# Performance work log

Hardware: AMD Instinct MI355X
Metric: run time of the kernel (lower is better)

The kernel has to match this reference:

```python
import jax, jax.numpy as jnp
import numpy as np

N_STEP = 64
GAMMA = 10.0
DIST_MIN, DIST_MAX = 0.0, 10.0
N_LAYER = 4
H_DIM, E_DIM, HID_DIM = 128, 16, 256
N_NODES, N_EDGES = 10000, 320000


def setup_inputs() -> dict:
    key = jax.random.key(0)
    ks = jax.random.split(key, 12)
    in_m = 2 * H_DIM + E_DIM + N_STEP  # 336
    s = 0.02
    return {
        "x": jax.random.normal(ks[0], (N_NODES, H_DIM), jnp.float32),
        "pos": jax.random.normal(ks[1], (N_NODES, 3), jnp.float32),
        "edge_index": jax.random.randint(ks[2], (2, N_EDGES), 0, N_NODES),
        "edge_attr": jax.random.normal(ks[3], (N_EDGES, E_DIM), jnp.float32),
        "Wm": jax.random.normal(ks[4], (N_LAYER, in_m, HID_DIM), jnp.float32) * s,
        "bm": jnp.zeros((N_LAYER, HID_DIM), jnp.float32),
        "Wp": jax.random.normal(ks[5], (N_LAYER, HID_DIM, 1), jnp.float32) * s,
        "bp": jnp.zeros((N_LAYER, 1), jnp.float32),
        "Wx": jax.random.normal(ks[6], (N_LAYER, H_DIM + HID_DIM, H_DIM), jnp.float32) * s,
        "bx": jnp.zeros((N_LAYER, H_DIM), jnp.float32),
    }


def _egnn_layer(x, pos, edge_index, edge_attr, Wm, bm, Wp, bp, Wx, bx):
    i, j = edge_index[0], edge_index[1]
    n = x.shape[0]
    x_i, x_j = x[i], x[j]                       # [E, h] gathers
    # NOTE: source uses x (not pos) for the distance feature -- replicated.
    r = jnp.linalg.norm(x_i - x_j, axis=1)      # [E]
    c = jnp.linspace(DIST_MIN, DIST_MAX, N_STEP, dtype=x.dtype)
    soh = jnp.exp(-GAMMA * (r[:, None] - c[None, :]) ** 2)  # [E, n_step]
    m_ij = jnp.concatenate([x_i, x_j, soh, edge_attr], axis=1) @ Wm + bm  # [E, hid]
    _alpha = m_ij @ Wp + bp  # computed but unused in source's _update_pos
    # position update: scatter-mean of pos_i - pos_j over destination i
    pos_vect = pos[i] - pos[j]                  # [E, 3]
    cnt = jax.ops.segment_sum(jnp.ones((i.shape[0],), pos.dtype), i, num_segments=n)
    pos_aggr = jax.ops.segment_sum(pos_vect, i, num_segments=n) / jnp.maximum(cnt, 1.0)[:, None]
    pos = pos + pos_aggr
    # feature update: scatter-sum of messages
    m_aggr = jax.ops.segment_sum(m_ij, i, num_segments=n)  # [N, hid]
    x = jnp.concatenate([x, m_aggr], axis=1) @ Wx + bx      # [N, h]
    return x, pos


def reference(x, pos, edge_index, edge_attr, Wm, bm, Wp, bp, Wx, bx):
    x_ori = x
    for l in range(N_LAYER):
        x, pos = _egnn_layer(x, pos, edge_index, edge_attr,
                             Wm[l], bm[l], Wp[l], bp[l], Wx[l], bx[l])
        x = jax.nn.leaky_relu(x)
    x = x_ori + x            # residual_connection == 'add'
    x = jax.nn.leaky_relu(x)  # activate_last
    return x, pos
```

## Files before the change

### kernel.cpp

```cpp
#include <hip/hip_runtime.h>
#include <hip/hip_bf16.h>

#define NN 10000
#define NE 320000
#define HD 128
#define ED 16
#define HID 256
#define KP 480
#define AST 488

typedef unsigned short ushort_t;
typedef __attribute__((ext_vector_type(8))) short short8;
typedef __attribute__((ext_vector_type(4))) float f32x4;

__device__ __forceinline__ float leaky(float v){ return v > 0.f ? v : 0.01f*v; }
__device__ __forceinline__ ushort_t f2bs(float v){
  __hip_bfloat16 b = __float2bfloat16(v);
  return *(ushort_t*)&b;
}
__device__ __forceinline__ unsigned pack2u(float a, float b){
  return (unsigned)f2bs(a) | ((unsigned)f2bs(b) << 16);
}
__device__ __forceinline__ float bl(unsigned u){ return __uint_as_float(u << 16); }
__device__ __forceinline__ float bh(unsigned u){ return __uint_as_float(u & 0xffff0000u); }
__device__ __forceinline__ float2 cvt2(unsigned u){ return make_float2(bl(u), bh(u)); }

__global__ __launch_bounds__(256) void k_misc(const float* __restrict__ x, ushort_t* __restrict__ xb,
                                              const int* __restrict__ ii, int* __restrict__ cnt,
                                              const float* __restrict__ Wx, ushort_t* __restrict__ WcT){
  int t = blockIdx.x*256 + threadIdx.x;
  if (t < NN*HD){
    xb[t] = f2bs(x[t]);
  } else if (t < NN*HD + NE){
    atomicAdd(&cnt[ii[t - NN*HD]], 1);
  } else if (t < NN*HD + NE + 4*HD*HD){
    int u = t - NN*HD - NE;
    int l = u >> 14, r = (u >> 7) & 127, c = u & 127;
    WcT[((long)l*HD + c)*KP + r] = f2bs(Wx[(long)l*(HD+HID)*HD + r*HD + c]);
  } else {
    int u = t - NN*HD - NE - 4*HD*HD;
    if (u < 4*HD*15){
      int row = u / 15, k = 465 + u % 15;
      WcT[(long)row*KP + k] = 0;
    }
  }
}

__global__ __launch_bounds__(256) void k_scan(const int* __restrict__ cnt, int* __restrict__ row_ptr){
  const int PER = 40;
  __shared__ int sh[256];
  int t = threadIdx.x;
  int base = t*PER;
  int s = 0;
  for (int k = 0; k < PER; ++k){ int idx = base+k; if (idx < NN) s += cnt[idx]; }
  sh[t] = s; __syncthreads();
  for (int off = 1; off < 256; off <<= 1){
    int v = (t >= off) ? sh[t-off] : 0;
    __syncthreads();
    sh[t] += v;
    __syncthreads();
  }
  int pre = sh[t] - s;
  for (int k = 0; k < PER; ++k){
    int idx = base+k;
    if (idx < NN){ row_ptr[idx] = pre; pre += cnt[idx]; }
  }
  if (t == 255) row_ptr[NN] = sh[255];
}

__global__ __launch_bounds__(256) void k_fillwc(const int* __restrict__ ii, const int* __restrict__ jj,
                                                const int* __restrict__ row_ptr, int* __restrict__ c2,
                                                int* __restrict__ sj, int* __restrict__ se,
                                                const float* __restrict__ Wm, const float* __restrict__ bm,
                                                const float* __restrict__ Wx, ushort_t* __restrict__ WcT){
  if (blockIdx.x < 1250){
    int e = blockIdx.x*256 + threadIdx.x;
    int a = ii[e];
    int p = atomicAdd(&c2[a], 1);
    int idx = row_ptr[a] + p;
    sj[idx] = jj[e];
    se[idx] = e;
    return;
  }
  __shared__ float a_s[16*36];
  __shared__ float w_s[16*128];
  int bi = blockIdx.x - 1250;
  int t  = threadIdx.x;
  int rb = (bi % 11) * 32;
  int l  = bi / 11;
  int lr = t >> 4, lk = t & 15;
  int wcc = t & 127, wk = t >> 7;
  int cg = t & 31, rg = t >> 5;
  const float* Wxb = Wx + (long)l*(HD+HID)*HD + HD*HD;
  float acc[4][4];
  #pragma unroll
  for (int i = 0; i < 4; ++i)
    #pragma unroll
    for (int j = 0; j < 4; ++j) acc[i][j] = 0.f;
  for (int k0 = 0; k0 < HID; k0 += 16){
    int m0 = rb + lr, m1 = rb + lr + 16;
    float v0 = 0.f, v1 = 0.f;
    if (m0 < 336) v0 = Wm[((long)l*336 + m0)*HID + k0 + lk];
    else if (m0 == 336) v0 = bm[l*HID + k0 + lk];
    if (m1 < 336) v1 = Wm[((long)l*336 + m1)*HID + k0 + lk];
    else if (m1 == 336) v1 = bm[l*HID + k0 + lk];
    a_s[lk*36 + lr]      = v0;
    a_s[lk*36 + lr + 16] = v1;
    #pragma unroll
    for (int q = 0; q < 8; ++q)
      w_s[(wk + 2*q)*128 + wcc] = Wxb[(k0 + wk + 2*q)*HD + wcc];
    __syncthreads();
    #pragma unroll
    for (int k = 0; k < 16; ++k){
      float4 av = *(const float4*)&a_s[k*36 + rg*4];
      float4 wv = *(const float4*)&w_s[k*128 + cg*4];
      acc[0][0] += av.x*wv.x; acc[0][1] += av.x*wv.y; acc[0][2] += av.x*wv.z; acc[0][3] += av.x*wv.w;
      acc[1][0] += av.y*wv.x; acc[1][1] += av.y*wv.y; acc[1][2] += av.y*wv.z; acc[1][3] += av.y*wv.w;
      acc[2][0] += av.z*wv.x; acc[2][1] += av.z*wv.y; acc[2][2] += av.z*wv.z; acc[2][3] += av.z*wv.w;
      acc[3][0] += av.w*wv.x; acc[3][1] += av.w*wv.y; acc[3][2] += av.w*wv.z; acc[3][3] += av.w*wv.w;
    }
    __syncthreads();
  }
  #pragma unroll
  for (int i = 0; i < 4; ++i){
    int m = rb + rg*4 + i;
    if (m < 337){
      #pragma unroll
      for (int j = 0; j < 4; ++j)
        WcT[((long)l*HD + cg*4 + j)*KP + 128 + m] = f2bs(acc[i][j]);
    }
  }
}

template<int FIRST, int FINAL>
__global__ __launch_bounds__(256) void k_layer(const uint4* __restrict__ xb4, const float* __restrict__ posf_cur,
                                               const int* __restrict__ row_ptr, const int* __restrict__ sj,
                                               const int* __restrict__ se, const float* __restrict__ ea,
                                               ushort_t* __restrict__ inv,
                                               const ushort_t* __restrict__ WcT, const float* __restrict__ bx,
                                               ushort_t* __restrict__ xb_next, const float* __restrict__ x_ori,
                                               float* __restrict__ out, float* __restrict__ posf_next){
  __shared__ ushort_t Asm[8*AST];
  int tid = threadIdx.x;
  int nl  = tid >> 5;
  int n   = blockIdx.x*8 + nl;
  int sub = tid & 31;
  int g   = sub >> 4;
  int gl  = sub & 15;
  int beg = row_ptr[n], end = row_ptr[n+1];
  int len = end - beg;
  int q0 = beg + ((len * g) >> 1);
  int q1 = beg + ((len * (g+1)) >> 1);

  uint4 xi = xb4[(long)n*16 + gl];
  float2 xi0 = cvt2(xi.x), xi1 = cvt2(xi.y), xi2 = cvt2(xi.z), xi3 = cvt2(xi.w);
  float c0 = (10.0f/63.0f)*(float)(4*gl);
  float c1 = (10.0f/63.0f)*(float)(4*gl+1);
  float c2 = (10.0f/63.0f)*(float)(4*gl+2);
  float c3 = (10.0f/63.0f)*(float)(4*gl+3);

  float2 s0 = {0,0}, s1 = {0,0}, s2 = {0,0}, s3 = {0,0};
  float h0 = 0, h1 = 0, h2 = 0, h3 = 0, sp = 0, sea = 0;

#define EPROC(Bv, Jv, Ev) { \
    float2 e0=cvt2(Bv.x), e1=cvt2(Bv.y), e2=cvt2(Bv.z), e3=cvt2(Bv.w); \
    float d, p=0.f; \
    d=xi0.x-e0.x; p+=d*d;  d=xi0.y-e0.y; p+=d*d; \
    d=xi1.x-e1.x; p+=d*d;  d=xi1.y-e1.y; p+=d*d; \
    d=xi2.x-e2.x; p+=d*d;  d=xi2.y-e2.y; p+=d*d; \
    d=xi3.x-e3.x; p+=d*d;  d=xi3.y-e3.y; p+=d*d; \
    p += __shfl_xor(p,1,64); p += __shfl_xor(p,2,64); \
    p += __shfl_xor(p,4,64); p += __shfl_xor(p,8,64); \
    float r = sqrtf(p); \
    float t0=r-c0, t1=r-c1, t2=r-c2, t3=r-c3; \
    h0 += __expf(-10.f*t0*t0); h1 += __expf(-10.f*t1*t1); \
    h2 += __expf(-10.f*t2*t2); h3 += __expf(-10.f*t3*t3); \
    s0.x+=e0.x; s0.y+=e0.y; s1.x+=e1.x; s1.y+=e1.y; \
    s2.x+=e2.x; s2.y+=e2.y; s3.x+=e3.x; s3.y+=e3.y; \
    if (FIRST) sea += ea[(long)(Ev)*ED + gl]; \
    if (gl < 3) sp += posf_cur[(long)Jv*3 + gl]; }

  int idx = q0;
  for (; idx + 3 < q1; idx += 4){
    int j0 = sj[idx], j1 = sj[idx+1], j2 = sj[idx+2], j3 = sj[idx+3];
    int e0i = FIRST ? se[idx]   : 0;
    int e1i = FIRST ? se[idx+1] : 0;
    int e2i = FIRST ? se[idx+2] : 0;
    int e3i = FIRST ? se[idx+3] : 0;
    uint4 B0 = xb4[(long)j0*16 + gl];
    uint4 B1 = xb4[(long)j1*16 + gl];
    uint4 B2 = xb4[(long)j2*16 + gl];
    uint4 B3 = xb4[(long)j3*16 + gl];
    EPROC(B0, j0, e0i); EPROC(B1, j1, e1i); EPROC(B2, j2, e2i); EPROC(B3, j3, e3i);
  }
  for (; idx < q1; ++idx){
    int j0 = sj[idx];
    int e0i = FIRST ? se[idx] : 0;
    uint4 B0 = xb4[(long)j0*16 + gl];
    EPROC(B0, j0, e0i);
  }
#undef EPROC

  s0.x += __shfl_xor(s0.x,16,64); s0.y += __shfl_xor(s0.y,16,64);
  s1.x += __shfl_xor(s1.x,16,64); s1.y += __shfl_xor(s1.y,16,64);
  s2.x += __shfl_xor(s2.x,16,64); s2.y += __shfl_xor(s2.y,16,64);
  s3.x += __shfl_xor(s3.x,16,64); s3.y += __shfl_xor(s3.y,16,64);
  h0 += __shfl_xor(h0,16,64); h1 += __shfl_xor(h1,16,64);
  h2 += __shfl_xor(h2,16,64); h3 += __shfl_xor(h3,16,64);
  sp += __shfl_xor(sp,16,64);
  if (FIRST) sea += __shfl_xor(sea,16,64);

  if (g == 0){
    float cf = (float)len;
    ushort_t* Ar = Asm + nl*AST;
    ((uint4*)Ar)[gl] = xi;
    ((uint4*)(Ar + 128))[gl] = make_uint4(pack2u(cf*xi0.x, cf*xi0.y), pack2u(cf*xi1.x, cf*xi1.y),
                                          pack2u(cf*xi2.x, cf*xi2.y), pack2u(cf*xi3.x, cf*xi3.y));
    ((uint4*)(Ar + 256))[gl] = make_uint4(pack2u(s0.x, s0.y), pack2u(s1.x, s1.y),
                                          pack2u(s2.x, s2.y), pack2u(s3.x, s3.y));
    ((uint2*)(Ar + 384))[gl] = make_uint2(pack2u(h0, h1), pack2u(h2, h3));
    ushort_t sea_us;
    if (FIRST){
      sea_us = f2bs(sea);
      inv[(long)n*16 + gl] = sea_us;
    } else {
      sea_us = inv[(long)n*16 + gl];
    }
    Ar[448 + gl] = sea_us;
    Ar[464 + gl] = (gl == 0) ? f2bs(cf) : (ushort_t)0;
    if (gl < 3){
      float pi = posf_cur[n*3 + gl];
      posf_next[n*3 + gl] = pi + (cf*pi - sp) / fmaxf(cf, 1.f);
    }
  }
  __syncthreads();

  int wave = tid >> 6, lane = tid & 63;
  int quad = lane >> 4, l16 = lane & 15;
  int nb = wave * 32;
  const ushort_t* Arow = Asm + (l16 & 7)*AST + quad*8;
  const ushort_t* W0 = WcT + (long)(nb + l16)*KP + quad*8;
  const ushort_t* W1 = WcT + (long)(nb + 16 + l16)*KP + quad*8;
  f32x4 acc0 = {0,0,0,0}, acc1 = {0,0,0,0};
  for (int k0 = 0; k0 < KP; k0 += 32){
    short8 av = *(const short8*)(Arow + k0);
    short8 b0 = *(const short8*)(W0 + k0);
    short8 b1 = *(const short8*)(W1 + k0);
    acc0 = __builtin_amdgcn_mfma_f32_16x16x32_bf16(av, b0, acc0, 0, 0, 0);
    acc1 = __builtin_amdgcn_mfma_f32_16x16x32_bf16(av, b1, acc1, 0, 0, 0);
  }
  float bx0 = bx[nb + l16], bx1 = bx[nb + 16 + l16];
  #pragma unroll
  for (int r = 0; r < 4; ++r){
    int row = quad*4 + r;
    if (row < 8){
      long base = (long)(blockIdx.x*8 + row)*HD;
      float v0 = leaky(acc0[r] + bx0);
      float v1 = leaky(acc1[r] + bx1);
      if (FINAL){
        out[base + nb + l16]      = leaky(x_ori[base + nb + l16] + v0);
        out[base + nb + 16 + l16] = leaky(x_ori[base + nb + 16 + l16] + v1);
      } else {
        xb_next[base + nb + l16]      = f2bs(v0);
        xb_next[base + nb + 16 + l16] = f2bs(v1);
      }
    }
  }
}

extern "C" void kernel_launch(void* const* d_in, const int* in_sizes, int n_in,
                              void* d_out, int out_size, void* d_ws, size_t ws_size,
                              hipStream_t stream){
  const float* x   = (const float*)d_in[0];
  const float* pos = (const float*)d_in[1];
  const int*   ei  = (const int*)d_in[2];
  const float* ea  = (const float*)d_in[3];
  const float* Wm  = (const float*)d_in[4];
  const float* bm  = (const float*)d_in[5];
  const float* Wx  = (const float*)d_in[8];
  const float* bx  = (const float*)d_in[9];
  float* out_x   = (float*)d_out;
  float* out_pos = out_x + NN*HD;

  ushort_t* xbA    = (ushort_t*)d_ws;
  ushort_t* xbB    = xbA + NN*HD;
  ushort_t* WcT    = xbB + NN*HD;
  ushort_t* inv    = WcT + 4*HD*KP;
  float*    pfA    = (float*)(inv + NN*16);
  float*    pfB    = pfA + NN*3;
  int*      cnt    = (int*)(pfB + NN*3);
  int*      c2     = cnt + NN;
  int*      row_ptr= c2 + NN;
  int*      sj     = row_ptr + (NN+1);
  int*      se     = sj + NE;
  const int* ii = ei;
  const int* jj = ei + NE;

  hipMemsetAsync(cnt, 0, 2*NN*sizeof(int), stream);
  int misc_threads = NN*HD + NE + 4*HD*HD + 4*HD*15;
  k_misc  <<<(misc_threads + 255)/256, 256, 0, stream>>>(x, xbA, ii, cnt, Wx, WcT);
  k_scan  <<<1, 256, 0, stream>>>(cnt, row_ptr);
  k_fillwc<<<1250 + 44, 256, 0, stream>>>(ii, jj, row_ptr, c2, sj, se, Wm, bm, Wx, WcT);

  const float* ps[4] = {pos, pfA, pfB, pfA};
  float*       pd[4] = {pfA, pfB, pfA, out_pos};

  k_layer<1,0><<<1250, 256, 0, stream>>>((const uint4*)xbA, ps[0], row_ptr, sj, se, ea, inv,
                                         WcT + 0*HD*KP, bx + 0*HD, xbB, x, out_x, pd[0]);
  k_layer<0,0><<<1250, 256, 0, stream>>>((const uint4*)xbB, ps[1], row_ptr, sj, se, ea, inv,
                                         WcT + 1*(long)HD*KP, bx + 1*HD, xbA, x, out_x, pd[1]);
  k_layer<0,0><<<1250, 256, 0, stream>>>((const uint4*)xbA, ps[2], row_ptr, sj, se, ea, inv,
                                         WcT + 2*(long)HD*KP, bx + 2*HD, xbB, x, out_x, pd[2]);
  k_layer<0,1><<<1250, 256, 0, stream>>>((const uint4*)xbB, ps[3], row_ptr, sj, se, ea, inv,
                                         WcT + 3*(long)HD*KP, bx + 3*HD, xbA, x, out_x, pd[3]);
}
```

Measured before the change: 333.0 us.

## Give each node a full wavefront and pack CSR neighbor/edge ids together

Each node's edge list is now split across four 16-lane groups, so one 64-lane wavefront handles one node (4 nodes per block, 2500 blocks) instead of two groups per node. The aim is more parallelism per node to hide gather latency on the degree-32 neighbor lists. The CSR fill now reuses the rank returned by the counting atomic, which removes the second atomic pass and the c2 counter. Neighbor and edge ids are stored as an int2 pair so one load fetches both. In exchange, the MFMA stage uses only 4 of its 16 rows, so half as many nodes share each weight read and more weight traffic falls on each block.

```diff
diff --git a/kernel.cpp b/kernel.cpp
--- a/kernel.cpp
+++ b/kernel.cpp
@@ -27,12 +27,14 @@
 
 __global__ __launch_bounds__(256) void k_misc(const float* __restrict__ x, ushort_t* __restrict__ xb,
                                               const int* __restrict__ ii, int* __restrict__ cnt,
+                                              int* __restrict__ rank,
                                               const float* __restrict__ Wx, ushort_t* __restrict__ WcT){
   int t = blockIdx.x*256 + threadIdx.x;
   if (t < NN*HD){
     xb[t] = f2bs(x[t]);
   } else if (t < NN*HD + NE){
-    atomicAdd(&cnt[ii[t - NN*HD]], 1);
+    int e = t - NN*HD;
+    rank[e] = atomicAdd(&cnt[ii[e]], 1);
   } else if (t < NN*HD + NE + 4*HD*HD){
     int u = t - NN*HD - NE;
     int l = u >> 14, r = (u >> 7) & 127, c = u & 127;
@@ -69,17 +71,14 @@
 }
 
 __global__ __launch_bounds__(256) void k_fillwc(const int* __restrict__ ii, const int* __restrict__ jj,
-                                                const int* __restrict__ row_ptr, int* __restrict__ c2,
-                                                int* __restrict__ sj, int* __restrict__ se,
+                                                const int* __restrict__ row_ptr, const int* __restrict__ rank,
+                                                int2* __restrict__ sje,
                                                 const float* __restrict__ Wm, const float* __restrict__ bm,
                                                 const float* __restrict__ Wx, ushort_t* __restrict__ WcT){
   if (blockIdx.x < 1250){
     int e = blockIdx.x*256 + threadIdx.x;
     int a = ii[e];
-    int p = atomicAdd(&c2[a], 1);
-    int idx = row_ptr[a] + p;
-    sj[idx] = jj[e];
-    se[idx] = e;
+    sje[row_ptr[a] + rank[e]] = make_int2(jj[e], e);
     return;
   }
   __shared__ float a_s[16*36];
@@ -134,23 +133,23 @@
 
 template<int FIRST, int FINAL>
 __global__ __launch_bounds__(256) void k_layer(const uint4* __restrict__ xb4, const float* __restrict__ posf_cur,
-                                               const int* __restrict__ row_ptr, const int* __restrict__ sj,
-                                               const int* __restrict__ se, const float* __restrict__ ea,
+                                               const int* __restrict__ row_ptr, const int2* __restrict__ sje,
+                                               const float* __restrict__ ea,
                                                ushort_t* __restrict__ inv,
                                                const ushort_t* __restrict__ WcT, const float* __restrict__ bx,
                                                ushort_t* __restrict__ xb_next, const float* __restrict__ x_ori,
                                                float* __restrict__ out, float* __restrict__ posf_next){
-  __shared__ ushort_t Asm[8*AST];
-  int tid = threadIdx.x;
-  int nl  = tid >> 5;
-  int n   = blockIdx.x*8 + nl;
-  int sub = tid & 31;
-  int g   = sub >> 4;
-  int gl  = sub & 15;
+  __shared__ ushort_t Asm[4*AST];
+  int tid  = threadIdx.x;
+  int nl   = tid >> 6;
+  int n    = blockIdx.x*4 + nl;
+  int lane = tid & 63;
+  int g    = lane >> 4;
+  int gl   = lane & 15;
   int beg = row_ptr[n], end = row_ptr[n+1];
   int len = end - beg;
-  int q0 = beg + ((len * g) >> 1);
-  int q1 = beg + ((len * (g+1)) >> 1);
+  int q0 = beg + ((len * g) >> 2);
+  int q1 = beg + ((len * (g+1)) >> 2);
 
   uint4 xi = xb4[(long)n*16 + gl];
   float2 xi0 = cvt2(xi.x), xi1 = cvt2(xi.y), xi2 = cvt2(xi.z), xi3 = cvt2(xi.w);
@@ -178,39 +177,33 @@
     s0.x+=e0.x; s0.y+=e0.y; s1.x+=e1.x; s1.y+=e1.y; \
     s2.x+=e2.x; s2.y+=e2.y; s3.x+=e3.x; s3.y+=e3.y; \
     if (FIRST) sea += ea[(long)(Ev)*ED + gl]; \
-    if (gl < 3) sp += posf_cur[(long)Jv*3 + gl]; }
+    if (gl < 3) sp += posf_cur[(long)(Jv)*3 + gl]; }
 
   int idx = q0;
   for (; idx + 3 < q1; idx += 4){
-    int j0 = sj[idx], j1 = sj[idx+1], j2 = sj[idx+2], j3 = sj[idx+3];
-    int e0i = FIRST ? se[idx]   : 0;
-    int e1i = FIRST ? se[idx+1] : 0;
-    int e2i = FIRST ? se[idx+2] : 0;
-    int e3i = FIRST ? se[idx+3] : 0;
-    uint4 B0 = xb4[(long)j0*16 + gl];
-    uint4 B1 = xb4[(long)j1*16 + gl];
-    uint4 B2 = xb4[(long)j2*16 + gl];
-    uint4 B3 = xb4[(long)j3*16 + gl];
-    EPROC(B0, j0, e0i); EPROC(B1, j1, e1i); EPROC(B2, j2, e2i); EPROC(B3, j3, e3i);
+    int2 p0 = sje[idx], p1 = sje[idx+1], p2 = sje[idx+2], p3 = sje[idx+3];
+    uint4 B0 = xb4[(long)p0.x*16 + gl];
+    uint4 B1 = xb4[(long)p1.x*16 + gl];
+    uint4 B2 = xb4[(long)p2.x*16 + gl];
+    uint4 B3 = xb4[(long)p3.x*16 + gl];
+    EPROC(B0, p0.x, p0.y); EPROC(B1, p1.x, p1.y); EPROC(B2, p2.x, p2.y); EPROC(B3, p3.x, p3.y);
   }
   for (; idx < q1; ++idx){
-    int j0 = sj[idx];
-    int e0i = FIRST ? se[idx] : 0;
-    uint4 B0 = xb4[(long)j0*16 + gl];
-    EPROC(B0, j0, e0i);
+    int2 p0 = sje[idx];
+    uint4 B0 = xb4[(long)p0.x*16 + gl];
+    EPROC(B0, p0.x, p0.y);
   }
 #undef EPROC
 
-  s0.x += __shfl_xor(s0.x,16,64); s0.y += __shfl_xor(s0.y,16,64);
-  s1.x += __shfl_xor(s1.x,16,64); s1.y += __shfl_xor(s1.y,16,64);
-  s2.x += __shfl_xor(s2.x,16,64); s2.y += __shfl_xor(s2.y,16,64);
-  s3.x += __shfl_xor(s3.x,16,64); s3.y += __shfl_xor(s3.y,16,64);
-  h0 += __shfl_xor(h0,16,64); h1 += __shfl_xor(h1,16,64);
-  h2 += __shfl_xor(h2,16,64); h3 += __shfl_xor(h3,16,64);
-  sp += __shfl_xor(sp,16,64);
-  if (FIRST) sea += __shfl_xor(sea,16,64);
-
-  if (g == 0){
+#define RED2(v) { v += __shfl_xor(v,16,64); v += __shfl_xor(v,32,64); }
+  RED2(s0.x) RED2(s0.y) RED2(s1.x) RED2(s1.y)
+  RED2(s2.x) RED2(s2.y) RED2(s3.x) RED2(s3.y)
+  RED2(h0) RED2(h1) RED2(h2) RED2(h3)
+  RED2(sp)
+  if (FIRST) { RED2(sea) }
+#undef RED2
+
+  if (lane < 16){
     float cf = (float)len;
     ushort_t* Ar = Asm + nl*AST;
     ((uint4*)Ar)[gl] = xi;
@@ -235,10 +228,10 @@
   }
   __syncthreads();
 
-  int wave = tid >> 6, lane = tid & 63;
+  int wave = tid >> 6;
   int quad = lane >> 4, l16 = lane & 15;
   int nb = wave * 32;
-  const ushort_t* Arow = Asm + (l16 & 7)*AST + quad*8;
+  const ushort_t* Arow = Asm + (l16 & 3)*AST + quad*8;
   const ushort_t* W0 = WcT + (long)(nb + l16)*KP + quad*8;
   const ushort_t* W1 = WcT + (long)(nb + 16 + l16)*KP + quad*8;
   f32x4 acc0 = {0,0,0,0}, acc1 = {0,0,0,0};
@@ -253,8 +246,8 @@
   #pragma unroll
   for (int r = 0; r < 4; ++r){
     int row = quad*4 + r;
-    if (row < 8){
-      long base = (long)(blockIdx.x*8 + row)*HD;
+    if (row < 4){
+      long base = (long)(blockIdx.x*4 + row)*HD;
       float v0 = leaky(acc0[r] + bx0);
       float v1 = leaky(acc1[r] + bx1);
       if (FINAL){
@@ -289,28 +282,27 @@
   float*    pfA    = (float*)(inv + NN*16);
   float*    pfB    = pfA + NN*3;
   int*      cnt    = (int*)(pfB + NN*3);
-  int*      c2     = cnt + NN;
-  int*      row_ptr= c2 + NN;
-  int*      sj     = row_ptr + (NN+1);
-  int*      se     = sj + NE;
+  int*      row_ptr= cnt + NN;
+  int2*     sje    = (int2*)(row_ptr + (NN+2));
+  int*      rank   = (int*)xbB;
   const int* ii = ei;
   const int* jj = ei + NE;
 
-  hipMemsetAsync(cnt, 0, 2*NN*sizeof(int), stream);
+  hipMemsetAsync(cnt, 0, NN*sizeof(int), stream);
   int misc_threads = NN*HD + NE + 4*HD*HD + 4*HD*15;
-  k_misc  <<<(misc_threads + 255)/256, 256, 0, stream>>>(x, xbA, ii, cnt, Wx, WcT);
+  k_misc  <<<(misc_threads + 255)/256, 256, 0, stream>>>(x, xbA, ii, cnt, rank, Wx, WcT);
   k_scan  <<<1, 256, 0, stream>>>(cnt, row_ptr);
-  k_fillwc<<<1250 + 44, 256, 0, stream>>>(ii, jj, row_ptr, c2, sj, se, Wm, bm, Wx, WcT);
+  k_fillwc<<<1250 + 44, 256, 0, stream>>>(ii, jj, row_ptr, rank, sje, Wm, bm, Wx, WcT);
 
   const float* ps[4] = {pos, pfA, pfB, pfA};
   float*       pd[4] = {pfA, pfB, pfA, out_pos};
 
-  k_layer<1,0><<<1250, 256, 0, stream>>>((const uint4*)xbA, ps[0], row_ptr, sj, se, ea, inv,
+  k_layer<1,0><<<2500, 256, 0, stream>>>((const uint4*)xbA, ps[0], row_ptr, sje, ea, inv,
                                          WcT + 0*HD*KP, bx + 0*HD, xbB, x, out_x, pd[0]);
-  k_layer<0,0><<<1250, 256, 0, stream>>>((const uint4*)xbB, ps[1], row_ptr, sj, se, ea, inv,
+  k_layer<0,0><<<2500, 256, 0, stream>>>((const uint4*)xbB, ps[1], row_ptr, sje, ea, inv,
                                          WcT + 1*(long)HD*KP, bx + 1*HD, xbA, x, out_x, pd[1]);
-  k_layer<0,0><<<1250, 256, 0, stream>>>((const uint4*)xbA, ps[2], row_ptr, sj, se, ea, inv,
+  k_layer<0,0><<<2500, 256, 0, stream>>>((const uint4*)xbA, ps[2], row_ptr, sje, ea, inv,
                                          WcT + 2*(long)HD*KP, bx + 2*HD, xbB, x, out_x, pd[2]);
-  k_layer<0,1><<<1250, 256, 0, stream>>>((const uint4*)xbB, ps[3], row_ptr, sj, se, ea, inv,
+  k_layer<0,1><<<2500, 256, 0, stream>>>((const uint4*)xbB, ps[3], row_ptr, sje, ea, inv,
                                          WcT + 3*(long)HD*KP, bx + 3*HD, xbA, x, out_x, pd[3]);
 }
```

New measurement: 336.3 us. Within noise of the previous version (+1.0%).

## Stage neighbor lists in LDS and software-pipeline gathers in edge loop

Applied to the files above, without the earlier changes.

Each node's (neighbor, edge) pairs are interleaved into one int2 CSR array and loaded cooperatively into shared memory, up to 64 per node. The edge loop is restructured into double-buffered groups of four, issuing the next group's feature gathers before computing the current group and batching the shuffle reductions. CSR construction now records each edge's atomic rank during counting, which removes the second atomic pass and its counter array. The bf16 conversion is vectorised to eight elements per thread. This adds register pressure and shared memory use, and degrees above 64 fall back to a slower unpipelined path.

```diff
diff --git a/kernel.cpp b/kernel.cpp
--- a/kernel.cpp
+++ b/kernel.cpp
@@ -27,18 +27,24 @@
 
 __global__ __launch_bounds__(256) void k_misc(const float* __restrict__ x, ushort_t* __restrict__ xb,
                                               const int* __restrict__ ii, int* __restrict__ cnt,
+                                              int* __restrict__ rank,
                                               const float* __restrict__ Wx, ushort_t* __restrict__ WcT){
   int t = blockIdx.x*256 + threadIdx.x;
-  if (t < NN*HD){
-    xb[t] = f2bs(x[t]);
-  } else if (t < NN*HD + NE){
-    atomicAdd(&cnt[ii[t - NN*HD]], 1);
-  } else if (t < NN*HD + NE + 4*HD*HD){
-    int u = t - NN*HD - NE;
+  const int S0 = NN*HD/8;
+  if (t < S0){
+    float4 a = ((const float4*)x)[2*t];
+    float4 b = ((const float4*)x)[2*t+1];
+    ((uint4*)xb)[t] = make_uint4(pack2u(a.x,a.y), pack2u(a.z,a.w),
+                                 pack2u(b.x,b.y), pack2u(b.z,b.w));
+  } else if (t < S0 + NE){
+    int e = t - S0;
+    rank[e] = atomicAdd(&cnt[ii[e]], 1);
+  } else if (t < S0 + NE + 4*HD*HD){
+    int u = t - S0 - NE;
     int l = u >> 14, r = (u >> 7) & 127, c = u & 127;
     WcT[((long)l*HD + c)*KP + r] = f2bs(Wx[(long)l*(HD+HID)*HD + r*HD + c]);
   } else {
-    int u = t - NN*HD - NE - 4*HD*HD;
+    int u = t - S0 - NE - 4*HD*HD;
     if (u < 4*HD*15){
       int row = u / 15, k = 465 + u % 15;
       WcT[(long)row*KP + k] = 0;
@@ -69,17 +75,14 @@
 }
 
 __global__ __launch_bounds__(256) void k_fillwc(const int* __restrict__ ii, const int* __restrict__ jj,
-                                                const int* __restrict__ row_ptr, int* __restrict__ c2,
-                                                int* __restrict__ sj, int* __restrict__ se,
+                                                const int* __restrict__ row_ptr, const int* __restrict__ rank,
+                                                int2* __restrict__ sje,
                                                 const float* __restrict__ Wm, const float* __restrict__ bm,
                                                 const float* __restrict__ Wx, ushort_t* __restrict__ WcT){
   if (blockIdx.x < 1250){
     int e = blockIdx.x*256 + threadIdx.x;
     int a = ii[e];
-    int p = atomicAdd(&c2[a], 1);
-    int idx = row_ptr[a] + p;
-    sj[idx] = jj[e];
-    se[idx] = e;
+    sje[row_ptr[a] + rank[e]] = make_int2(jj[e], e);
     return;
   }
   __shared__ float a_s[16*36];
@@ -134,13 +137,14 @@
 
 template<int FIRST, int FINAL>
 __global__ __launch_bounds__(256) void k_layer(const uint4* __restrict__ xb4, const float* __restrict__ posf_cur,
-                                               const int* __restrict__ row_ptr, const int* __restrict__ sj,
-                                               const int* __restrict__ se, const float* __restrict__ ea,
+                                               const int* __restrict__ row_ptr, const int2* __restrict__ sje,
+                                               const float* __restrict__ ea,
                                                ushort_t* __restrict__ inv,
                                                const ushort_t* __restrict__ WcT, const float* __restrict__ bx,
                                                ushort_t* __restrict__ xb_next, const float* __restrict__ x_ori,
                                                float* __restrict__ out, float* __restrict__ posf_next){
   __shared__ ushort_t Asm[8*AST];
+  __shared__ int2 sjL[8][64];
   int tid = threadIdx.x;
   int nl  = tid >> 5;
   int n   = blockIdx.x*8 + nl;
@@ -149,8 +153,11 @@
   int gl  = sub & 15;
   int beg = row_ptr[n], end = row_ptr[n+1];
   int len = end - beg;
-  int q0 = beg + ((len * g) >> 1);
-  int q1 = beg + ((len * (g+1)) >> 1);
+  int len2 = len < 64 ? len : 64;
+
+  if (sub < len2)       sjL[nl][sub]      = sje[beg + sub];
+  if (sub + 32 < len2)  sjL[nl][sub + 32] = sje[beg + sub + 32];
+  __builtin_amdgcn_wave_barrier();
 
   uint4 xi = xb4[(long)n*16 + gl];
   float2 xi0 = cvt2(xi.x), xi1 = cvt2(xi.y), xi2 = cvt2(xi.z), xi3 = cvt2(xi.w);
@@ -162,44 +169,99 @@
   float2 s0 = {0,0}, s1 = {0,0}, s2 = {0,0}, s3 = {0,0};
   float h0 = 0, h1 = 0, h2 = 0, h3 = 0, sp = 0, sea = 0;
 
-#define EPROC(Bv, Jv, Ev) { \
+#define DPART(Bv, P) { \
     float2 e0=cvt2(Bv.x), e1=cvt2(Bv.y), e2=cvt2(Bv.z), e3=cvt2(Bv.w); \
-    float d, p=0.f; \
-    d=xi0.x-e0.x; p+=d*d;  d=xi0.y-e0.y; p+=d*d; \
-    d=xi1.x-e1.x; p+=d*d;  d=xi1.y-e1.y; p+=d*d; \
-    d=xi2.x-e2.x; p+=d*d;  d=xi2.y-e2.y; p+=d*d; \
-    d=xi3.x-e3.x; p+=d*d;  d=xi3.y-e3.y; p+=d*d; \
-    p += __shfl_xor(p,1,64); p += __shfl_xor(p,2,64); \
-    p += __shfl_xor(p,4,64); p += __shfl_xor(p,8,64); \
-    float r = sqrtf(p); \
+    float d, q=0.f; \
+    d=xi0.x-e0.x; q+=d*d;  d=xi0.y-e0.y; q+=d*d; \
+    d=xi1.x-e1.x; q+=d*d;  d=xi1.y-e1.y; q+=d*d; \
+    d=xi2.x-e2.x; q+=d*d;  d=xi2.y-e2.y; q+=d*d; \
+    d=xi3.x-e3.x; q+=d*d;  d=xi3.y-e3.y; q+=d*d; \
+    s0.x+=e0.x; s0.y+=e0.y; s1.x+=e1.x; s1.y+=e1.y; \
+    s2.x+=e2.x; s2.y+=e2.y; s3.x+=e3.x; s3.y+=e3.y; \
+    P = q; }
+
+#define HPART(P) { \
+    float r = sqrtf(P); \
     float t0=r-c0, t1=r-c1, t2=r-c2, t3=r-c3; \
     h0 += __expf(-10.f*t0*t0); h1 += __expf(-10.f*t1*t1); \
-    h2 += __expf(-10.f*t2*t2); h3 += __expf(-10.f*t3*t3); \
-    s0.x+=e0.x; s0.y+=e0.y; s1.x+=e1.x; s1.y+=e1.y; \
-    s2.x+=e2.x; s2.y+=e2.y; s3.x+=e3.x; s3.y+=e3.y; \
-    if (FIRST) sea += ea[(long)(Ev)*ED + gl]; \
-    if (gl < 3) sp += posf_cur[(long)Jv*3 + gl]; }
-
-  int idx = q0;
-  for (; idx + 3 < q1; idx += 4){
-    int j0 = sj[idx], j1 = sj[idx+1], j2 = sj[idx+2], j3 = sj[idx+3];
-    int e0i = FIRST ? se[idx]   : 0;
-    int e1i = FIRST ? se[idx+1] : 0;
-    int e2i = FIRST ? se[idx+2] : 0;
-    int e3i = FIRST ? se[idx+3] : 0;
-    uint4 B0 = xb4[(long)j0*16 + gl];
-    uint4 B1 = xb4[(long)j1*16 + gl];
-    uint4 B2 = xb4[(long)j2*16 + gl];
-    uint4 B3 = xb4[(long)j3*16 + gl];
-    EPROC(B0, j0, e0i); EPROC(B1, j1, e1i); EPROC(B2, j2, e2i); EPROC(B3, j3, e3i);
-  }
-  for (; idx < q1; ++idx){
-    int j0 = sj[idx];
-    int e0i = FIRST ? se[idx] : 0;
-    uint4 B0 = xb4[(long)j0*16 + gl];
-    EPROC(B0, j0, e0i);
-  }
-#undef EPROC
+    h2 += __expf(-10.f*t2*t2); h3 += __expf(-10.f*t3*t3); }
+
+#define LOADB(Bx, jx, ex, off) { \
+    int2 a0 = sjL[nl][(off)], a1 = sjL[nl][(off)+1], a2 = sjL[nl][(off)+2], a3 = sjL[nl][(off)+3]; \
+    jx[0]=a0.x; jx[1]=a1.x; jx[2]=a2.x; jx[3]=a3.x; \
+    if (FIRST){ ex[0]=a0.y; ex[1]=a1.y; ex[2]=a2.y; ex[3]=a3.y; } \
+    Bx[0] = xb4[(long)a0.x*16 + gl]; \
+    Bx[1] = xb4[(long)a1.x*16 + gl]; \
+    Bx[2] = xb4[(long)a2.x*16 + gl]; \
+    Bx[3] = xb4[(long)a3.x*16 + gl]; }
+
+#define COMPUTE(Bx, jx, ex) { \
+    float w0=0,w1=0,w2=0,w3=0; \
+    if (gl < 3){ \
+      w0 = posf_cur[(long)jx[0]*3 + gl]; w1 = posf_cur[(long)jx[1]*3 + gl]; \
+      w2 = posf_cur[(long)jx[2]*3 + gl]; w3 = posf_cur[(long)jx[3]*3 + gl]; } \
+    float y0=0,y1=0,y2=0,y3=0; \
+    if (FIRST){ \
+      y0 = ea[(long)ex[0]*ED + gl]; y1 = ea[(long)ex[1]*ED + gl]; \
+      y2 = ea[(long)ex[2]*ED + gl]; y3 = ea[(long)ex[3]*ED + gl]; } \
+    float p0_,p1_,p2_,p3_; \
+    DPART(Bx[0], p0_) DPART(Bx[1], p1_) DPART(Bx[2], p2_) DPART(Bx[3], p3_) \
+    p0_ += __shfl_xor(p0_,1,64); p1_ += __shfl_xor(p1_,1,64); p2_ += __shfl_xor(p2_,1,64); p3_ += __shfl_xor(p3_,1,64); \
+    p0_ += __shfl_xor(p0_,2,64); p1_ += __shfl_xor(p1_,2,64); p2_ += __shfl_xor(p2_,2,64); p3_ += __shfl_xor(p3_,2,64); \
+    p0_ += __shfl_xor(p0_,4,64); p1_ += __shfl_xor(p1_,4,64); p2_ += __shfl_xor(p2_,4,64); p3_ += __shfl_xor(p3_,4,64); \
+    p0_ += __shfl_xor(p0_,8,64); p1_ += __shfl_xor(p1_,8,64); p2_ += __shfl_xor(p2_,8,64); p3_ += __shfl_xor(p3_,8,64); \
+    HPART(p0_) HPART(p1_) HPART(p2_) HPART(p3_) \
+    sp += (w0+w1)+(w2+w3); \
+    if (FIRST) sea += (y0+y1)+(y2+y3); }
+
+#define EP1(Jv, Ev) { \
+    uint4 Bv = xb4[(long)(Jv)*16 + gl]; \
+    float wv = 0; if (gl < 3) wv = posf_cur[(long)(Jv)*3 + gl]; \
+    float yv = 0; if (FIRST) yv = ea[(long)(Ev)*ED + gl]; \
+    float pv; DPART(Bv, pv) \
+    pv += __shfl_xor(pv,1,64); pv += __shfl_xor(pv,2,64); \
+    pv += __shfl_xor(pv,4,64); pv += __shfl_xor(pv,8,64); \
+    HPART(pv) \
+    sp += wv; if (FIRST) sea += yv; }
+
+  int lo   = g ? (len2 >> 1) : 0;
+  int hi   = g ? len2 : (len2 >> 1);
+  int cntg = hi - lo;
+  int nb4  = cntg >> 2;
+
+  uint4 BA[4], BB_[4];
+  int jA[4], jB[4], eA[4], eB[4];
+  (void)eA; (void)eB;
+  if (nb4 > 0){
+    LOADB(BA, jA, eA, lo)
+    int b = 1;
+    for (; b + 1 < nb4; b += 2){
+      LOADB(BB_, jB, eB, lo + 4*b)
+      COMPUTE(BA, jA, eA)
+      LOADB(BA, jA, eA, lo + 4*b + 4)
+      COMPUTE(BB_, jB, eB)
+    }
+    if (b < nb4){
+      LOADB(BB_, jB, eB, lo + 4*b)
+      COMPUTE(BA, jA, eA)
+      COMPUTE(BB_, jB, eB)
+    } else {
+      COMPUTE(BA, jA, eA)
+    }
+  }
+  for (int k = lo + (nb4 << 2); k < hi; ++k){
+    int2 pr = sjL[nl][k];
+    EP1(pr.x, pr.y)
+  }
+  for (int q2 = 64 + g; q2 < len; q2 += 2){
+    int2 pr = sje[beg + q2];
+    EP1(pr.x, pr.y)
+  }
+#undef DPART
+#undef HPART
+#undef LOADB
+#undef COMPUTE
+#undef EP1
 
   s0.x += __shfl_xor(s0.x,16,64); s0.y += __shfl_xor(s0.y,16,64);
   s1.x += __shfl_xor(s1.x,16,64); s1.y += __shfl_xor(s1.y,16,64);
@@ -289,28 +351,27 @@
   float*    pfA    = (float*)(inv + NN*16);
   float*    pfB    = pfA + NN*3;
   int*      cnt    = (int*)(pfB + NN*3);
-  int*      c2     = cnt + NN;
-  int*      row_ptr= c2 + NN;
-  int*      sj     = row_ptr + (NN+1);
-  int*      se     = sj + NE;
+  int*      row_ptr= cnt + NN;
+  int2*     sje    = (int2*)(row_ptr + (NN+2));
+  int*      rank   = (int*)xbB;
   const int* ii = ei;
   const int* jj = ei + NE;
 
-  hipMemsetAsync(cnt, 0, 2*NN*sizeof(int), stream);
-  int misc_threads = NN*HD + NE + 4*HD*HD + 4*HD*15;
-  k_misc  <<<(misc_threads + 255)/256, 256, 0, stream>>>(x, xbA, ii, cnt, Wx, WcT);
+  hipMemsetAsync(cnt, 0, NN*sizeof(int), stream);
+  int misc_threads = NN*HD/8 + NE + 4*HD*HD + 4*HD*15;
+  k_misc  <<<(misc_threads + 255)/256, 256, 0, stream>>>(x, xbA, ii, cnt, rank, Wx, WcT);
   k_scan  <<<1, 256, 0, stream>>>(cnt, row_ptr);
-  k_fillwc<<<1250 + 44, 256, 0, stream>>>(ii, jj, row_ptr, c2, sj, se, Wm, bm, Wx, WcT);
+  k_fillwc<<<1250 + 44, 256, 0, stream>>>(ii, jj, row_ptr, rank, sje, Wm, bm, Wx, WcT);
 
   const float* ps[4] = {pos, pfA, pfB, pfA};
   float*       pd[4] = {pfA, pfB, pfA, out_pos};
 
-  k_layer<1,0><<<1250, 256, 0, stream>>>((const uint4*)xbA, ps[0], row_ptr, sj, se, ea, inv,
+  k_layer<1,0><<<1250, 256, 0, stream>>>((const uint4*)xbA, ps[0], row_ptr, sje, ea, inv,
                                          WcT + 0*HD*KP, bx + 0*HD, xbB, x, out_x, pd[0]);
-  k_layer<0,0><<<1250, 256, 0, stream>>>((const uint4*)xbB, ps[1], row_ptr, sj, se, ea, inv,
+  k_layer<0,0><<<1250, 256, 0, stream>>>((const uint4*)xbB, ps[1], row_ptr, sje, ea, inv,
                                          WcT + 1*(long)HD*KP, bx + 1*HD, xbA, x, out_x, pd[1]);
-  k_layer<0,0><<<1250, 256, 0, stream>>>((const uint4*)xbA, ps[2], row_ptr, sj, se, ea, inv,
+  k_layer<0,0><<<1250, 256, 0, stream>>>((const uint4*)xbA, ps[2], row_ptr, sje, ea, inv,
                                          WcT + 2*(long)HD*KP, bx + 2*HD, xbB, x, out_x, pd[2]);
-  k_layer<0,1><<<1250, 256, 0, stream>>>((const uint4*)xbB, ps[3], row_ptr, sj, se, ea, inv,
+  k_layer<0,1><<<1250, 256, 0, stream>>>((const uint4*)xbB, ps[3], row_ptr, sje, ea, inv,
                                          WcT + 3*(long)HD*KP, bx + 3*HD, xbA, x, out_x, pd[3]);
 }
```

New measurement: 308.2 us. 1.08x faster.
